# Performance work log

Hardware: AMD Instinct MI355X
Metric: run time of the kernel (lower is better)

## Reference

```python
import jax, jax.numpy as jnp
import numpy as np
import math

N_EMBD = 1024
N_HEAD = 16
HEAD_DIM = N_EMBD // N_HEAD
SEQ = 2048
BATCH = 2
EPS = 1e-5


def _gelu_tanh(x):
    c = math.sqrt(2.0 / math.pi)
    return 0.5 * x * (1.0 + jnp.tanh(c * (x + 0.044715 * x ** 3)))


def _layernorm(x, w, b):
    mean = jnp.mean(x, axis=-1, keepdims=True)
    var = jnp.mean(jnp.square(x - mean), axis=-1, keepdims=True)  # unbiased=False
    return (x - mean) / jnp.sqrt(var + EPS) * w + b


def setup_inputs() -> dict:
    key = jax.random.key(0)
    ks = jax.random.split(key, 8)
    D = N_EMBD
    s = 0.02
    return {
        "x": jax.random.normal(ks[0], (BATCH, SEQ, D), jnp.float32),
        "ln1_w": jnp.ones((D,), jnp.float32),
        "ln1_b": jnp.zeros((D,), jnp.float32),
        "w_qkv": jax.random.normal(ks[1], (D, 3 * D), jnp.float32) * s,
        "b_qkv": jnp.zeros((3 * D,), jnp.float32),
        "w_attn_proj": jax.random.normal(ks[2], (D, D), jnp.float32) * s,
        "b_attn_proj": jnp.zeros((D,), jnp.float32),
        "ln2_w": jnp.ones((D,), jnp.float32),
        "ln2_b": jnp.zeros((D,), jnp.float32),
        "w_fc": jax.random.normal(ks[3], (D, 4 * D), jnp.float32) * s,
        "b_fc": jnp.zeros((4 * D,), jnp.float32),
        "w_proj": jax.random.normal(ks[4], (4 * D, D), jnp.float32) * s,
        "b_proj": jnp.zeros((D,), jnp.float32),
    }


def reference(x, ln1_w, ln1_b, w_qkv, b_qkv, w_attn_proj, b_attn_proj,
              ln2_w, ln2_b, w_fc, b_fc, w_proj, b_proj):
    bs, T, D = x.shape
    # --- attention branch (pre-LN) ---
    h = _layernorm(x, ln1_w, ln1_b)
    qkv = h @ w_qkv + b_qkv                      # [B,T,3D]
    q, k, v = jnp.split(qkv, 3, axis=-1)
    q = q.reshape(bs, T, N_HEAD, HEAD_DIM).transpose(0, 2, 1, 3)  # [B,H,T,d]
    k = k.reshape(bs, T, N_HEAD, HEAD_DIM).transpose(0, 2, 1, 3)
    v = v.reshape(bs, T, N_HEAD, HEAD_DIM).transpose(0, 2, 1, 3)
    scores = jnp.einsum("bhqd,bhkd->bhqk", q, k) * (1.0 / math.sqrt(HEAD_DIM))
    causal = jnp.tril(jnp.ones((T, T), bool))
    scores = jnp.where(causal[None, None], scores, -jnp.inf)
    att = jax.nn.softmax(scores, axis=-1)
    ctx = jnp.einsum("bhqk,bhkd->bhqd", att, v)
    ctx = ctx.transpose(0, 2, 1, 3).reshape(bs, T, D)
    attn_out = ctx @ w_attn_proj + b_attn_proj
    x = x + attn_out
    # --- MLP branch (pre-LN) ---
    h = _layernorm(x, ln2_w, ln2_b)
    h = _gelu_tanh(h @ w_fc + b_fc)
    h = h @ w_proj + b_proj
    return x + h
```

## Files before the change

### kernel.cpp

```cpp
#include <hip/hip_runtime.h>

typedef unsigned short u16;
typedef __attribute__((ext_vector_type(8))) __bf16 bf16x8;
typedef __attribute__((ext_vector_type(8))) unsigned short ushort8;
typedef __attribute__((ext_vector_type(4))) float f32x4;

#define MFMA16(a, b, c) __builtin_amdgcn_mfma_f32_16x16x32_bf16((a), (b), (c), 0, 0, 0)

__device__ __forceinline__ u16 f2bf(float f) {
  union { __bf16 h; u16 u; } cv;
  cv.h = (__bf16)f;
  return cv.u;
}

__device__ __forceinline__ void async16(const u16* g, u16* l) {
  __builtin_amdgcn_global_load_lds(
      (const __attribute__((address_space(1))) void*)g,
      (__attribute__((address_space(3))) void*)l, 16, 0, 0);
}

__global__ __launch_bounds__(256)
void transpose_bf16(const float* __restrict__ W, u16* __restrict__ Wt, int K, int N) {
  __shared__ float t[32][33];
  const int n0 = blockIdx.x * 32, k0 = blockIdx.y * 32;
  const int tx = threadIdx.x, ty = threadIdx.y;
  #pragma unroll
  for (int i = 0; i < 32; i += 8)
    t[ty + i][tx] = W[(size_t)(k0 + ty + i) * N + n0 + tx];
  __syncthreads();
  #pragma unroll
  for (int i = 0; i < 32; i += 8)
    Wt[(size_t)(n0 + ty + i) * K + k0 + tx] = f2bf(t[tx][ty + i]);
}

__global__ __launch_bounds__(256)
void transpose_v(const u16* __restrict__ v, u16* __restrict__ vt) {
  __shared__ u16 t[64][72];
  const int bh = blockIdx.y, t0 = blockIdx.x * 64;
  const int tid = threadIdx.x;
  #pragma unroll
  for (int s = 0; s < 2; ++s) {
    const int idx = tid + s * 256;
    const int row = idx >> 3, ch = idx & 7;
    ushort8 d = *(const ushort8*)(v + ((size_t)bh * 2048 + t0 + row) * 64 + ch * 8);
    #pragma unroll
    for (int e = 0; e < 8; ++e) t[ch * 8 + e][row] = d[e];
  }
  __syncthreads();
  #pragma unroll
  for (int s = 0; s < 2; ++s) {
    const int idx = tid + s * 256;
    const int drow = idx >> 3, ch = idx & 7;
    ushort8 o = *(const ushort8*)(&t[drow][ch * 8]);
    *(ushort8*)(vt + ((size_t)bh * 64 + drow) * 2048 + t0 + ch * 8) = o;
  }
}

__global__ __launch_bounds__(256)
void ln_bf16(const float* __restrict__ X, const float* __restrict__ w,
             const float* __restrict__ bia, u16* __restrict__ out) {
  const int row = blockIdx.x, tid = threadIdx.x;
  const float4 v = ((const float4*)(X + (size_t)row * 1024))[tid];
  float s = v.x + v.y + v.z + v.w;
  float s2 = v.x * v.x + v.y * v.y + v.z * v.z + v.w * v.w;
  #pragma unroll
  for (int o = 32; o > 0; o >>= 1) { s += __shfl_down(s, o); s2 += __shfl_down(s2, o); }
  __shared__ float red[8];
  const int wv = tid >> 6, lane = tid & 63;
  if (lane == 0) { red[wv] = s; red[4 + wv] = s2; }
  __syncthreads();
  s = red[0] + red[1] + red[2] + red[3];
  s2 = red[4] + red[5] + red[6] + red[7];
  const float mean = s * (1.f / 1024.f);
  const float var = s2 * (1.f / 1024.f) - mean * mean;
  const float rstd = rsqrtf(var + 1e-5f);
  const float4 wv4 = ((const float4*)w)[tid];
  const float4 bv4 = ((const float4*)bia)[tid];
  ushort4 o;
  o.x = f2bf((v.x - mean) * rstd * wv4.x + bv4.x);
  o.y = f2bf((v.y - mean) * rstd * wv4.y + bv4.y);
  o.z = f2bf((v.z - mean) * rstd * wv4.z + bv4.z);
  o.w = f2bf((v.w - mean) * rstd * wv4.w + bv4.w);
  ((ushort4*)(out + (size_t)row * 1024))[tid] = o;
}

template <int MODE>
__global__ __launch_bounds__(256)
void gemm_bt(const u16* __restrict__ A, const u16* __restrict__ Bt,
             const float* __restrict__ bias, const float* __restrict__ resid,
             float* __restrict__ outF, u16* __restrict__ outB,
             u16* __restrict__ qo, u16* __restrict__ ko, u16* __restrict__ vo,
             int M, int N, int K, int kSlice) {
  __shared__ u16 As[128 * 64];
  __shared__ u16 Bs[128 * 64];
  const int tid = threadIdx.x;
  const int lane = tid & 63, wv = tid >> 6;
  const int l16 = lane & 15, quad = lane >> 4;
  const int wr = wv >> 1, wc = wv & 1;
  const int m0 = blockIdx.y * 128, n0 = blockIdx.x * 128;
  const int kBegin = blockIdx.z * kSlice, kEnd = kBegin + kSlice;
  const int srow = lane >> 3;
  const int sch = (lane & 7) ^ srow;

  f32x4 acc[4][4];
  const f32x4 fz = {0.f, 0.f, 0.f, 0.f};
  #pragma unroll
  for (int i = 0; i < 4; ++i)
    #pragma unroll
    for (int j = 0; j < 4; ++j) acc[i][j] = fz;

  for (int k0 = kBegin; k0 < kEnd; k0 += 64) {
    __syncthreads();
    #pragma unroll
    for (int s = 0; s < 4; ++s) {
      const int R = wv * 32 + s * 8;
      async16(A + (size_t)(m0 + R + srow) * K + k0 + sch * 8, As + R * 64);
      async16(Bt + (size_t)(n0 + R + srow) * K + k0 + sch * 8, Bs + R * 64);
    }
    __builtin_amdgcn_s_waitcnt(0xF70);
    __syncthreads();
    #pragma unroll
    for (int h = 0; h < 2; ++h) {
      bf16x8 af[4], bfr[4];
      #pragma unroll
      for (int i = 0; i < 4; ++i) {
        const int row = wr * 64 + i * 16 + l16;
        af[i] = *(const bf16x8*)(As + row * 64 + (((h * 4 + quad) ^ (l16 & 7)) * 8));
      }
      #pragma unroll
      for (int j = 0; j < 4; ++j) {
        const int row = wc * 64 + j * 16 + l16;
        bfr[j] = *(const bf16x8*)(Bs + row * 64 + (((h * 4 + quad) ^ (l16 & 7)) * 8));
      }
      #pragma unroll
      for (int i = 0; i < 4; ++i)
        #pragma unroll
        for (int j = 0; j < 4; ++j)
          acc[i][j] = MFMA16(af[i], bfr[j], acc[i][j]);
    }
  }

  #pragma unroll
  for (int i = 0; i < 4; ++i) {
    #pragma unroll
    for (int j = 0; j < 4; ++j) {
      const int col = n0 + wc * 64 + j * 16 + l16;
      #pragma unroll
      for (int r = 0; r < 4; ++r) {
        const int row = m0 + wr * 64 + i * 16 + quad * 4 + r;
        outF[(size_t)blockIdx.z * M * N + (size_t)row * N + col] = acc[i][j][r];
      }
    }
  }
}

template <int MODE>
__global__ __launch_bounds__(512, 2)
void gemm256(const u16* __restrict__ A, const u16* __restrict__ Bt,
             const float* __restrict__ bias, u16* __restrict__ outB,
             u16* __restrict__ qo, u16* __restrict__ ko, u16* __restrict__ vo,
             int M, int N, int K) {
  __shared__ u16 As[2][256 * 64];
  __shared__ u16 Bs[2][256 * 64];
  const int tid = threadIdx.x;
  const int lane = tid & 63, wv = tid >> 6;
  const int l16 = lane & 15, quad = lane >> 4;
  const int wr = wv >> 2, wc = wv & 3;
  const int nwg = gridDim.x, cpx = nwg >> 3;
  const int bid = (int)blockIdx.x;
  const int swz = (bid & 7) * cpx + (bid >> 3);
  const int nbx = N >> 8;
  const int m0 = (swz / nbx) * 256, n0 = (swz % nbx) * 256;
  const int sRow = lane >> 3;
  const int sCh = (lane & 7) ^ (sRow & 7);

  f32x4 acc[8][4];
  const f32x4 fz = {0.f, 0.f, 0.f, 0.f};
  #pragma unroll
  for (int i = 0; i < 8; ++i)
    #pragma unroll
    for (int j = 0; j < 4; ++j) acc[i][j] = fz;

  auto stageA = [&](int kt, int p) {
    const u16* g = A + (size_t)(m0 + wv * 8 + sRow) * K + kt * 64 + sCh * 8;
    u16* l = &As[p][(wv * 8) * 64];
    #pragma unroll
    for (int i = 0; i < 4; ++i)
      async16(g + (size_t)(i * 64) * K, l + i * 64 * 64);
  };
  auto stageB = [&](int kt, int p) {
    const u16* g = Bt + (size_t)(n0 + wv * 8 + sRow) * K + kt * 64 + sCh * 8;
    u16* l = &Bs[p][(wv * 8) * 64];
    #pragma unroll
    for (int i = 0; i < 4; ++i)
      async16(g + (size_t)(i * 64) * K, l + i * 64 * 64);
  };
  auto ldfrag = [&](const u16* base, int row, int sel) {
    return *(const bf16x8*)(base + row * 64 + ((sel ^ (row & 7)) * 8));
  };

  const int nt = K >> 6;
  stageA(0, 0);
  stageB(0, 0);
  __builtin_amdgcn_s_waitcnt(0xF70);
  __syncthreads();

  for (int kt = 0; kt < nt; ++kt) {
    const int p = kt & 1;
    const u16* Ap = As[p];
    const u16* Bp = Bs[p];
    const bool more = (kt + 1 < nt);
    bf16x8 a[4], b0[4], b1[4];

    if (more) stageA(kt + 1, p ^ 1);
    #pragma unroll
    for (int i = 0; i < 4; ++i) a[i] = ldfrag(Ap, wr * 128 + i * 16 + l16, quad);
    #pragma unroll
    for (int j = 0; j < 4; ++j) b0[j] = ldfrag(Bp, wc * 64 + j * 16 + l16, quad);
    __builtin_amdgcn_s_setprio(1);
    #pragma unroll
    for (int i = 0; i < 4; ++i)
      #pragma unroll
      for (int j = 0; j < 4; ++j) acc[i][j] = MFMA16(a[i], b0[j], acc[i][j]);
    __builtin_amdgcn_s_setprio(0);
    __builtin_amdgcn_s_barrier();

    if (more) stageB(kt + 1, p ^ 1);
    #pragma unroll
    for (int i = 0; i < 4; ++i) a[i] = ldfrag(Ap, wr * 128 + (4 + i) * 16 + l16, quad);
    __builtin_amdgcn_s_setprio(1);
    #pragma unroll
    for (int i = 0; i < 4; ++i)
      #pragma unroll
      for (int j = 0; j < 4; ++j) acc[4 + i][j] = MFMA16(a[i], b0[j], acc[4 + i][j]);
    __builtin_amdgcn_s_setprio(0);
    __builtin_amdgcn_s_barrier();

    #pragma unroll
    for (int i = 0; i < 4; ++i) a[i] = ldfrag(Ap, wr * 128 + i * 16 + l16, 4 + quad);
    #pragma unroll
    for (int j = 0; j < 4; ++j) b1[j] = ldfrag(Bp, wc * 64 + j * 16 + l16, 4 + quad);
    __builtin_amdgcn_s_setprio(1);
    #pragma unroll
    for (int i = 0; i < 4; ++i)
      #pragma unroll
      for (int j = 0; j < 4; ++j) acc[i][j] = MFMA16(a[i], b1[j], acc[i][j]);
    __builtin_amdgcn_s_setprio(0);
    __builtin_amdgcn_s_barrier();

    #pragma unroll
    for (int i = 0; i < 4; ++i) a[i] = ldfrag(Ap, wr * 128 + (4 + i) * 16 + l16, 4 + quad);
    __builtin_amdgcn_s_setprio(1);
    #pragma unroll
    for (int i = 0; i < 4; ++i)
      #pragma unroll
      for (int j = 0; j < 4; ++j) acc[4 + i][j] = MFMA16(a[i], b1[j], acc[4 + i][j]);
    __builtin_amdgcn_s_setprio(0);
    if (more) {
      __builtin_amdgcn_s_waitcnt(0xF70);
      __builtin_amdgcn_s_barrier();
      __builtin_amdgcn_sched_barrier(0);
    }
  }

  #pragma unroll
  for (int i = 0; i < 8; ++i) {
    #pragma unroll
    for (int j = 0; j < 4; ++j) {
      const int col = n0 + wc * 64 + j * 16 + l16;
      const float bc = bias[col];
      #pragma unroll
      for (int r = 0; r < 4; ++r) {
        const int row = m0 + wr * 128 + i * 16 + quad * 4 + r;
        float v = acc[i][j][r] + bc;
        if (MODE == 0) {
          const int which = col >> 10, cc = col & 1023, hh = cc >> 6, dd = cc & 63;
          const int bb = row >> 11, t = row & 2047;
          const u16 bv = f2bf(v);
          const size_t o = ((size_t)(bb * 16 + hh) * 2048 + t) * 64 + dd;
          if (which == 0)
            qo[o] = bv;
          else if (which == 1)
            ko[o] = bv;
          else
            vo[o] = bv;
        } else {
          const float x3 = v * v * v;
          const float u = 0.7978845608028654f * (v + 0.044715f * x3);
          const float e = __expf(2.f * u);
          const float th = 1.f - 2.f / (e + 1.f);
          outB[(size_t)row * N + col] = f2bf(0.5f * v * (1.f + th));
        }
      }
    }
  }
}

__global__ __launch_bounds__(256)
void reduce2(const float* __restrict__ P, const float* __restrict__ resid,
             const float* __restrict__ bias, float* __restrict__ out, int MN, int N) {
  const int idx4 = blockIdx.x * 256 + threadIdx.x;
  const size_t s = (size_t)MN >> 2;
  const float4 a = ((const float4*)P)[idx4];
  const float4 b = ((const float4*)P)[idx4 + s];
  const float4 r = ((const float4*)resid)[idx4];
  const float4 bb = ((const float4*)bias)[idx4 & (N / 4 - 1)];
  float4 o;
  o.x = r.x + a.x + b.x + bb.x;
  o.y = r.y + a.y + b.y + bb.y;
  o.z = r.z + a.z + b.z + bb.z;
  o.w = r.w + a.w + b.w + bb.w;
  ((float4*)out)[idx4] = o;
}

__global__ __launch_bounds__(256)
void reduce2_ln(const float* __restrict__ P, const float* __restrict__ resid,
                const float* __restrict__ bias, const float* __restrict__ lw,
                const float* __restrict__ lb, float* __restrict__ out,
                u16* __restrict__ h2, int MN) {
  const int row = blockIdx.x, tid = threadIdx.x;
  const int idx4 = row * 256 + tid;
  const size_t s4 = (size_t)MN >> 2;
  const float4 a = ((const float4*)P)[idx4];
  const float4 b = ((const float4*)P)[idx4 + s4];
  const float4 r = ((const float4*)resid)[idx4];
  const float4 bb = ((const float4*)bias)[tid];
  float4 o;
  o.x = r.x + a.x + b.x + bb.x;
  o.y = r.y + a.y + b.y + bb.y;
  o.z = r.z + a.z + b.z + bb.z;
  o.w = r.w + a.w + b.w + bb.w;
  ((float4*)out)[idx4] = o;
  float s = o.x + o.y + o.z + o.w;
  float s2 = o.x * o.x + o.y * o.y + o.z * o.z + o.w * o.w;
  #pragma unroll
  for (int of = 32; of > 0; of >>= 1) { s += __shfl_down(s, of); s2 += __shfl_down(s2, of); }
  __shared__ float red[8];
  const int wv = tid >> 6, lane = tid & 63;
  if (lane == 0) { red[wv] = s; red[4 + wv] = s2; }
  __syncthreads();
  s = red[0] + red[1] + red[2] + red[3];
  s2 = red[4] + red[5] + red[6] + red[7];
  const float mean = s * (1.f / 1024.f);
  const float var = s2 * (1.f / 1024.f) - mean * mean;
  const float rstd = rsqrtf(var + 1e-5f);
  const float4 wv4 = ((const float4*)lw)[tid];
  const float4 bv4 = ((const float4*)lb)[tid];
  ushort4 ob;
  ob.x = f2bf((o.x - mean) * rstd * wv4.x + bv4.x);
  ob.y = f2bf((o.y - mean) * rstd * wv4.y + bv4.y);
  ob.z = f2bf((o.z - mean) * rstd * wv4.z + bv4.z);
  ob.w = f2bf((o.w - mean) * rstd * wv4.w + bv4.w);
  ((ushort4*)(h2 + (size_t)row * 1024))[tid] = ob;
}

__global__ __launch_bounds__(256)
void attn(const u16* __restrict__ Q, const u16* __restrict__ Kg,
          const u16* __restrict__ Vt, u16* __restrict__ ctx) {
  __shared__ u16 Ks[2][128 * 64];
  __shared__ u16 Vs[64 * 128];
  __shared__ u16 Ps[64 * 128];
  const int px = blockIdx.x;
  const int pair = px >> 1, half = px & 1;
  const int qt0 = pair, qt1 = 15 - pair;
  const int bh = blockIdx.y;
  const int b = bh >> 4, h = bh & 15;
  const int tid = threadIdx.x;
  const int lane = tid & 63, wv = tid >> 6;
  const int l16 = lane & 15, quad = lane >> 4;
  const int rb = half * 64 + wv * 16;
  const int row_local = wv * 16 + l16;
  const float S2 = 0.18033688011112042f;
  const u16* Qb = Q + (size_t)bh * 2048 * 64;
  const u16* Kb = Kg + (size_t)bh * 2048 * 64;
  const u16* Vb = Vt + (size_t)bh * 64 * 2048;

  bf16x8 qf[2][2];
  #pragma unroll
  for (int t = 0; t < 2; ++t)
    #pragma unroll
    for (int c = 0; c < 2; ++c)
      qf[t][c] = *(const bf16x8*)(Qb + (size_t)((t ? qt1 : qt0) * 128 + rb + l16) * 64 +
                                  c * 32 + quad * 8);

  f32x4 octx[2][4];
  const f32x4 fz = {0.f, 0.f, 0.f, 0.f};
  #pragma unroll
  for (int t = 0; t < 2; ++t)
    #pragma unroll
    for (int jd = 0; jd < 4; ++jd) octx[t][jd] = fz;
  float mi2[2] = {-1e30f, -1e30f};
  float li[2] = {0.f, 0.f};

  const int kRow = lane >> 3, kCh = (lane & 7) ^ ((lane >> 3) & 7);
  const int vRow = lane >> 4;
  auto stageK = [&](int kt, int buf) {
    #pragma unroll
    for (int s = 0; s < 4; ++s) {
      const int R = wv * 32 + s * 8;
      async16(Kb + (size_t)(kt * 128 + R + kRow) * 64 + kCh * 8, &Ks[buf][R * 64]);
    }
  };
  auto stageV = [&](int kt) {
    #pragma unroll
    for (int s = 0; s < 4; ++s) {
      const int D = wv * 16 + s * 4;
      const int dd = D + vRow;
      const int sch = (lane & 15) ^ (dd & 15);
      async16(Vb + (size_t)dd * 2048 + kt * 128 + sch * 8, &Vs[D * 128]);
    }
  };

  auto softmax_t = [&](int t, f32x4* sa, int kt, int qt) {
    if (kt == qt) {
      const int rg = rb + l16;
      #pragma unroll
      for (int j = 0; j < 8; ++j)
        #pragma unroll
        for (int r = 0; r < 4; ++r)
          if (j * 16 + quad * 4 + r > rg) sa[j][r] = -1e30f;
    }
    float mx = -1e30f;
    #pragma unroll
    for (int j = 0; j < 8; ++j)
      #pragma unroll
      for (int r = 0; r < 4; ++r) mx = fmaxf(mx, sa[j][r]);
    mx = fmaxf(mx, __shfl_xor(mx, 16));
    mx = fmaxf(mx, __shfl_xor(mx, 32));
    mx *= S2;
    const float mn = fmaxf(mi2[t], mx);
    const float al = __builtin_amdgcn_exp2f(mi2[t] - mn);
    mi2[t] = mn;
    float rs = 0.f;
    #pragma unroll
    for (int j = 0; j < 8; ++j) {
      ushort4 w4;
      float p0 = __builtin_amdgcn_exp2f(sa[j][0] * S2 - mn);
      float p1 = __builtin_amdgcn_exp2f(sa[j][1] * S2 - mn);
      float p2 = __builtin_amdgcn_exp2f(sa[j][2] * S2 - mn);
      float p3 = __builtin_amdgcn_exp2f(sa[j][3] * S2 - mn);
      rs += (p0 + p1) + (p2 + p3);
      w4.x = f2bf(p0); w4.y = f2bf(p1); w4.z = f2bf(p2); w4.w = f2bf(p3);
      const int c = 2 * j + (quad >> 1);
      *(ushort4*)(Ps + row_local * 128 + ((c ^ l16) * 8) + (quad & 1) * 4) = w4;
    }
    rs += __shfl_xor(rs, 16);
    rs += __shfl_xor(rs, 32);
    li[t] = li[t] * al + rs;
    #pragma unroll
    for (int r = 0; r < 4; ++r) {
      const float alr = __shfl(al, quad * 4 + r);
      #pragma unroll
      for (int jd = 0; jd < 4; ++jd) octx[t][jd][r] *= alr;
    }
  };
  auto pv_t = [&](int t) {
    #pragma unroll
    for (int c = 0; c < 4; ++c) {
      bf16x8 pf = *(const bf16x8*)(Ps + row_local * 128 + (((c * 4 + quad) ^ l16) * 8));
      #pragma unroll
      for (int jd = 0; jd < 4; ++jd) {
        const int dd = jd * 16 + l16;
        bf16x8 vf = *(const bf16x8*)(Vs + dd * 128 + (((c * 4 + quad) ^ (dd & 15)) * 8));
        octx[t][jd] = MFMA16(pf, vf, octx[t][jd]);
      }
    }
  };

  stageK(0, 0);
  __builtin_amdgcn_s_waitcnt(0xF70);
  __syncthreads();

  for (int kt = 0; kt <= qt1; ++kt) {
    const int cur = kt & 1;
    stageV(kt);
    if (kt < qt1) stageK(kt + 1, cur ^ 1);
    const bool both = (kt <= qt0);

    f32x4 sa0[8], sa1[8];
    const u16* KsC = Ks[cur];
    #pragma unroll
    for (int j = 0; j < 8; ++j) {
      const int key7 = l16 & 7;
      bf16x8 kf0 = *(const bf16x8*)(KsC + (16 * j + l16) * 64 + ((quad ^ key7) * 8));
      bf16x8 kf1 = *(const bf16x8*)(KsC + (16 * j + l16) * 64 + (((4 + quad) ^ key7) * 8));
      sa1[j] = MFMA16(kf1, qf[1][1], MFMA16(kf0, qf[1][0], fz));
      if (both) sa0[j] = MFMA16(kf1, qf[0][1], MFMA16(kf0, qf[0][0], fz));
    }

    if (both)
      softmax_t(0, sa0, kt, qt0);
    else
      softmax_t(1, sa1, kt, qt1);

    __builtin_amdgcn_s_waitcnt(0xF70);
    __syncthreads();

    if (both) {
      pv_t(0);
      softmax_t(1, sa1, kt, qt1);
      pv_t(1);
    } else {
      pv_t(1);
    }
    __syncthreads();
  }

  #pragma unroll
  for (int t = 0; t < 2; ++t) {
    const int qt = t ? qt1 : qt0;
    #pragma unroll
    for (int r = 0; r < 4; ++r) {
      const float lr = __builtin_amdgcn_rcpf(__shfl(li[t], quad * 4 + r));
      const int rowg = qt * 128 + rb + quad * 4 + r;
      #pragma unroll
      for (int jd = 0; jd < 4; ++jd) {
        const int col = h * 64 + jd * 16 + l16;
        ctx[((size_t)b * 2048 + rowg) * 1024 + col] = f2bf(octx[t][jd][r] * lr);
      }
    }
  }
}

extern "C" void kernel_launch(void* const* d_in, const int* in_sizes, int n_in,
                              void* d_out, int out_size, void* d_ws, size_t ws_size,
                              hipStream_t stream) {
  (void)in_sizes; (void)n_in; (void)out_size; (void)ws_size;
  const float* x      = (const float*)d_in[0];
  const float* ln1_w  = (const float*)d_in[1];
  const float* ln1_b  = (const float*)d_in[2];
  const float* w_qkv  = (const float*)d_in[3];
  const float* b_qkv  = (const float*)d_in[4];
  const float* w_attn = (const float*)d_in[5];
  const float* b_attn = (const float*)d_in[6];
  const float* ln2_w  = (const float*)d_in[7];
  const float* ln2_b  = (const float*)d_in[8];
  const float* w_fc   = (const float*)d_in[9];
  const float* b_fc   = (const float*)d_in[10];
  const float* w_proj = (const float*)d_in[11];
  const float* b_proj = (const float*)d_in[12];
  float* out = (float*)d_out;

  char* ws = (char*)d_ws;
  size_t off = 0;
  auto alloc = [&](size_t n) {
    char* p = ws + off;
    off += (n + 255) & ~(size_t)255;
    return p;
  };
  u16* h1     = (u16*)alloc(4096ull * 1024 * 2);
  u16* wqkvT  = (u16*)alloc(3072ull * 1024 * 2);
  u16* wattnT = (u16*)alloc(1024ull * 1024 * 2);
  u16* wfcT   = (u16*)alloc(4096ull * 1024 * 2);
  u16* wprojT = (u16*)alloc(1024ull * 4096 * 2);
  u16* q      = (u16*)alloc(4096ull * 1024 * 2);
  u16* k      = (u16*)alloc(4096ull * 1024 * 2);
  u16* vT     = (u16*)alloc(4096ull * 1024 * 2);
  u16* ctxb   = (u16*)alloc(4096ull * 1024 * 2);
  float* out1 = (float*)alloc(4096ull * 1024 * 4);
  u16* h2     = (u16*)alloc(4096ull * 1024 * 2);
  u16* fco    = (u16*)alloc(4096ull * 4096 * 2);

  u16* vtmp = ctxb;
  float* apP = (float*)fco;
  float* projP = (float*)q;

  const dim3 tb(32, 8);
  transpose_bf16<<<dim3(3072 / 32, 1024 / 32), tb, 0, stream>>>(w_qkv, wqkvT, 1024, 3072);
  transpose_bf16<<<dim3(1024 / 32, 1024 / 32), tb, 0, stream>>>(w_attn, wattnT, 1024, 1024);
  transpose_bf16<<<dim3(4096 / 32, 1024 / 32), tb, 0, stream>>>(w_fc, wfcT, 1024, 4096);
  transpose_bf16<<<dim3(1024 / 32, 4096 / 32), tb, 0, stream>>>(w_proj, wprojT, 4096, 1024);

  ln_bf16<<<4096, 256, 0, stream>>>(x, ln1_w, ln1_b, h1);

  gemm256<0><<<dim3(192), 512, 0, stream>>>(h1, wqkvT, b_qkv, nullptr, q, k, vtmp,
                                            4096, 3072, 1024);

  transpose_v<<<dim3(32, 32), 256, 0, stream>>>(vtmp, vT);

  attn<<<dim3(16, 32), 256, 0, stream>>>(q, k, vT, ctxb);

  gemm_bt<4><<<dim3(8, 32, 2), 256, 0, stream>>>(ctxb, wattnT, b_attn, nullptr, apP, nullptr,
                                                 nullptr, nullptr, nullptr, 4096, 1024, 1024, 512);
  reduce2_ln<<<4096, 256, 0, stream>>>(apP, x, b_attn, ln2_w, ln2_b, out1, h2, 4096 * 1024);

  gemm256<2><<<dim3(256), 512, 0, stream>>>(h2, wfcT, b_fc, fco, nullptr, nullptr, nullptr,
                                            4096, 4096, 1024);

  gemm_bt<4><<<dim3(8, 32, 2), 256, 0, stream>>>(fco, wprojT, b_proj, nullptr, projP, nullptr,
                                                 nullptr, nullptr, nullptr, 4096, 1024, 4096, 2048);

  reduce2<<<4096, 256, 0, stream>>>(projP, out1, b_proj, out, 4096 * 1024, 1024);
}
```

Baseline: 386.8 us.

## Restructure attention to 512-thread blocks with register-shuffled P and lazy rescale

Each attention block now has 8 waves and covers the full 128-row query tile pair, so every staged K/V tile is shared by twice as many rows and each wave issues half as many staging loads. The P matrix no longer goes through shared memory; it is rearranged into the MFMA A-operand layout with lane shuffles. The running-max rescale is skipped when the new max exceeds the old by at most 8 (in log2 units), and s_setprio raises wave priority around the MFMA sections. The grid has half as many blocks and each block holds more registers, which may reduce occupancy, and the lazy-max threshold lets unnormalized exponentials grow larger before rescaling.

```diff
diff --git a/kernel.cpp b/kernel.cpp
--- a/kernel.cpp
+++ b/kernel.cpp
@@ -354,22 +354,21 @@
   ((ushort4*)(h2 + (size_t)row * 1024))[tid] = ob;
 }
 
-__global__ __launch_bounds__(256)
+typedef union { bf16x8 v; unsigned d[4]; } PFU;
+
+__global__ __launch_bounds__(512, 2)
 void attn(const u16* __restrict__ Q, const u16* __restrict__ Kg,
           const u16* __restrict__ Vt, u16* __restrict__ ctx) {
   __shared__ u16 Ks[2][128 * 64];
   __shared__ u16 Vs[64 * 128];
-  __shared__ u16 Ps[64 * 128];
-  const int px = blockIdx.x;
-  const int pair = px >> 1, half = px & 1;
+  const int pair = blockIdx.x;
   const int qt0 = pair, qt1 = 15 - pair;
   const int bh = blockIdx.y;
   const int b = bh >> 4, h = bh & 15;
   const int tid = threadIdx.x;
   const int lane = tid & 63, wv = tid >> 6;
   const int l16 = lane & 15, quad = lane >> 4;
-  const int rb = half * 64 + wv * 16;
-  const int row_local = wv * 16 + l16;
+  const int rb = wv * 16;
   const float S2 = 0.18033688011112042f;
   const u16* Qb = Q + (size_t)bh * 2048 * 64;
   const u16* Kb = Kg + (size_t)bh * 2048 * 64;
@@ -389,29 +388,34 @@
   for (int t = 0; t < 2; ++t)
     #pragma unroll
     for (int jd = 0; jd < 4; ++jd) octx[t][jd] = fz;
-  float mi2[2] = {-1e30f, -1e30f};
+  float mi[2] = {-1e30f, -1e30f};
   float li[2] = {0.f, 0.f};
 
   const int kRow = lane >> 3, kCh = (lane & 7) ^ ((lane >> 3) & 7);
   const int vRow = lane >> 4;
   auto stageK = [&](int kt, int buf) {
     #pragma unroll
-    for (int s = 0; s < 4; ++s) {
-      const int R = wv * 32 + s * 8;
+    for (int s = 0; s < 2; ++s) {
+      const int R = wv * 16 + s * 8;
       async16(Kb + (size_t)(kt * 128 + R + kRow) * 64 + kCh * 8, &Ks[buf][R * 64]);
     }
   };
   auto stageV = [&](int kt) {
     #pragma unroll
-    for (int s = 0; s < 4; ++s) {
-      const int D = wv * 16 + s * 4;
+    for (int s = 0; s < 2; ++s) {
+      const int D = wv * 8 + s * 4;
       const int dd = D + vRow;
       const int sch = (lane & 15) ^ (dd & 15);
       async16(Vb + (size_t)dd * 2048 + kt * 128 + sch * 8, &Vs[D * 128]);
     }
   };
 
-  auto softmax_t = [&](int t, f32x4* sa, int kt, int qt) {
+  const int ps0 = l16 + 16 * (2 * (quad & 1) + (quad >> 1));
+  const int ps1 = ps0 ^ 16;
+  const bool qlo = (quad & 1) == 0;
+  const bool qh2 = (quad >> 1) == 0;
+
+  auto smx = [&](f32x4* sa, int t, int kt, int qt, PFU* pf) {
     if (kt == qt) {
       const int rg = rb + l16;
       #pragma unroll
@@ -420,51 +424,78 @@
         for (int r = 0; r < 4; ++r)
           if (j * 16 + quad * 4 + r > rg) sa[j][r] = -1e30f;
     }
-    float mx = -1e30f;
+    float mj[8];
     #pragma unroll
     for (int j = 0; j < 8; ++j)
-      #pragma unroll
-      for (int r = 0; r < 4; ++r) mx = fmaxf(mx, sa[j][r]);
+      mj[j] = fmaxf(fmaxf(sa[j][0], sa[j][1]), fmaxf(sa[j][2], sa[j][3]));
+    float mx = fmaxf(fmaxf(fmaxf(mj[0], mj[1]), fmaxf(mj[2], mj[3])),
+                     fmaxf(fmaxf(mj[4], mj[5]), fmaxf(mj[6], mj[7])));
     mx = fmaxf(mx, __shfl_xor(mx, 16));
     mx = fmaxf(mx, __shfl_xor(mx, 32));
     mx *= S2;
-    const float mn = fmaxf(mi2[t], mx);
-    const float al = __builtin_amdgcn_exp2f(mi2[t] - mn);
-    mi2[t] = mn;
-    float rs = 0.f;
+    const bool skip = (__all(mx - mi[t] <= 8.f) != 0);
+    float mn = mi[t];
+    float al = 1.f;
+    if (!skip) {
+      mn = fmaxf(mi[t], mx);
+      al = __builtin_amdgcn_exp2f(mi[t] - mn);
+      mi[t] = mn;
+    }
+    float r0 = 0.f, r1 = 0.f, r2 = 0.f, r3 = 0.f;
+    unsigned w01[8], w23[8];
     #pragma unroll
     for (int j = 0; j < 8; ++j) {
-      ushort4 w4;
-      float p0 = __builtin_amdgcn_exp2f(sa[j][0] * S2 - mn);
-      float p1 = __builtin_amdgcn_exp2f(sa[j][1] * S2 - mn);
-      float p2 = __builtin_amdgcn_exp2f(sa[j][2] * S2 - mn);
-      float p3 = __builtin_amdgcn_exp2f(sa[j][3] * S2 - mn);
-      rs += (p0 + p1) + (p2 + p3);
-      w4.x = f2bf(p0); w4.y = f2bf(p1); w4.z = f2bf(p2); w4.w = f2bf(p3);
-      const int c = 2 * j + (quad >> 1);
-      *(ushort4*)(Ps + row_local * 128 + ((c ^ l16) * 8) + (quad & 1) * 4) = w4;
-    }
+      const float p0 = __builtin_amdgcn_exp2f(sa[j][0] * S2 - mn);
+      const float p1 = __builtin_amdgcn_exp2f(sa[j][1] * S2 - mn);
+      const float p2 = __builtin_amdgcn_exp2f(sa[j][2] * S2 - mn);
+      const float p3 = __builtin_amdgcn_exp2f(sa[j][3] * S2 - mn);
+      r0 += p0; r1 += p1; r2 += p2; r3 += p3;
+      w01[j] = (unsigned)f2bf(p0) | ((unsigned)f2bf(p1) << 16);
+      w23[j] = (unsigned)f2bf(p2) | ((unsigned)f2bf(p3) << 16);
+    }
+    float rs = (r0 + r1) + (r2 + r3);
     rs += __shfl_xor(rs, 16);
     rs += __shfl_xor(rs, 32);
-    li[t] = li[t] * al + rs;
-    #pragma unroll
-    for (int r = 0; r < 4; ++r) {
-      const float alr = __shfl(al, quad * 4 + r);
-      #pragma unroll
-      for (int jd = 0; jd < 4; ++jd) octx[t][jd][r] *= alr;
-    }
-  };
-  auto pv_t = [&](int t) {
+    if (skip) {
+      li[t] += rs;
+    } else {
+      li[t] = li[t] * al + rs;
+      #pragma unroll
+      for (int r = 0; r < 4; ++r) {
+        const float alr = __shfl(al, quad * 4 + r);
+        #pragma unroll
+        for (int jd = 0; jd < 4; ++jd) octx[t][jd][r] *= alr;
+      }
+    }
     #pragma unroll
     for (int c = 0; c < 4; ++c) {
-      bf16x8 pf = *(const bf16x8*)(Ps + row_local * 128 + (((c * 4 + quad) ^ l16) * 8));
+      const unsigned a0 = qlo ? w01[2 * c] : w01[2 * c + 1];
+      const unsigned a1 = qlo ? w01[2 * c + 1] : w01[2 * c];
+      const unsigned b0 = qlo ? w23[2 * c] : w23[2 * c + 1];
+      const unsigned b1 = qlo ? w23[2 * c + 1] : w23[2 * c];
+      const unsigned r00 = (unsigned)__shfl((int)a0, ps0);
+      const unsigned r01 = (unsigned)__shfl((int)a1, ps1);
+      const unsigned r10 = (unsigned)__shfl((int)b0, ps0);
+      const unsigned r11 = (unsigned)__shfl((int)b1, ps1);
+      pf[c].d[0] = qh2 ? r00 : r01;
+      pf[c].d[2] = qh2 ? r01 : r00;
+      pf[c].d[1] = qh2 ? r10 : r11;
+      pf[c].d[3] = qh2 ? r11 : r10;
+    }
+  };
+
+  auto pv = [&](PFU* pf, f32x4* oc) {
+    __builtin_amdgcn_s_setprio(1);
+    #pragma unroll
+    for (int c = 0; c < 4; ++c) {
       #pragma unroll
       for (int jd = 0; jd < 4; ++jd) {
         const int dd = jd * 16 + l16;
         bf16x8 vf = *(const bf16x8*)(Vs + dd * 128 + (((c * 4 + quad) ^ (dd & 15)) * 8));
-        octx[t][jd] = MFMA16(pf, vf, octx[t][jd]);
+        oc[jd] = MFMA16(pf[c].v, vf, oc[jd]);
       }
     }
+    __builtin_amdgcn_s_setprio(0);
   };
 
   stageK(0, 0);
@@ -479,6 +510,7 @@
 
     f32x4 sa0[8], sa1[8];
     const u16* KsC = Ks[cur];
+    __builtin_amdgcn_s_setprio(1);
     #pragma unroll
     for (int j = 0; j < 8; ++j) {
       const int key7 = l16 & 7;
@@ -487,21 +519,23 @@
       sa1[j] = MFMA16(kf1, qf[1][1], MFMA16(kf0, qf[1][0], fz));
       if (both) sa0[j] = MFMA16(kf1, qf[0][1], MFMA16(kf0, qf[0][0], fz));
     }
-
+    __builtin_amdgcn_s_setprio(0);
+
+    PFU pf0[4], pf1[4];
     if (both)
-      softmax_t(0, sa0, kt, qt0);
+      smx(sa0, 0, kt, qt0, pf0);
     else
-      softmax_t(1, sa1, kt, qt1);
+      smx(sa1, 1, kt, qt1, pf1);
 
     __builtin_amdgcn_s_waitcnt(0xF70);
     __syncthreads();
 
     if (both) {
-      pv_t(0);
-      softmax_t(1, sa1, kt, qt1);
-      pv_t(1);
+      pv(pf0, octx[0]);
+      smx(sa1, 1, kt, qt1, pf1);
+      pv(pf1, octx[1]);
     } else {
-      pv_t(1);
+      pv(pf1, octx[1]);
     }
     __syncthreads();
   }
@@ -578,7 +612,7 @@
 
   transpose_v<<<dim3(32, 32), 256, 0, stream>>>(vtmp, vT);
 
-  attn<<<dim3(16, 32), 256, 0, stream>>>(q, k, vT, ctxb);
+  attn<<<dim3(8, 32), 512, 0, stream>>>(q, k, vT, ctxb);
 
   gemm_bt<4><<<dim3(8, 32, 2), 256, 0, stream>>>(ctxb, wattnT, b_attn, nullptr, apP, nullptr,
                                                  nullptr, nullptr, nullptr, 4096, 1024, 1024, 512);
```

New measurement: 451.0 us. +16.6%, slower.
